# Kernel tuning notes

Measured on AMD Instinct MI355X. Metric: run time of the kernel, lower is better.

## Reference

```python
import jax, jax.numpy as jnp
import numpy as np

K = 1.0          # manifold curvature parameter (Lorentz hyperboloid <x,x>_L = -K)
NUM_HEADS = 16
LN_EPS = 1e-5
MID_EPS = 1e-8


def add_time(space):
    # lift a space-like vector onto the hyperboloid: x0 = sqrt(||s||^2 + K)
    t = jnp.sqrt(jnp.sum(space * space, axis=-1, keepdims=True) + K)
    return jnp.concatenate([t, space], axis=-1)


def hlinear(x, W, b):
    # Lorentz linear: dense map on full ambient vector -> space part, recompute time
    return add_time(jnp.einsum('...d,od->...o', x, W) + b)


def hyp_layernorm(x, g, b):
    s = x[..., 1:]
    mu = jnp.mean(s, axis=-1, keepdims=True)
    var = jnp.mean((s - mu) ** 2, axis=-1, keepdims=True)
    s = (s - mu) * jax.lax.rsqrt(var + LN_EPS) * g + b
    return add_time(s)


def hyp_relu(x):
    return add_time(jax.nn.relu(x[..., 1:]))


def lorentz_norm(v):
    # sqrt(|<v,v>_L|) with clamp for numerical safety
    inner = -v[..., 0] ** 2 + jnp.sum(v[..., 1:] ** 2, axis=-1)
    return jnp.sqrt(jnp.maximum(jnp.abs(inner), MID_EPS))


def midpoint_pair(z, x):
    # manifold.midpoint(stack([z, x], dim=-2)).squeeze(): mean then project back
    ave = 0.5 * (z + x)
    return jnp.sqrt(K) * ave / lorentz_norm(ave)[..., None]


def attention(x, Wq, bq, Wk, bk, Wv, bv, Wo, bo):
    B, S, D = x.shape
    dim = D - 1
    H = NUM_HEADS
    dh = dim // H

    def split_heads(t):
        # drop time, split space into heads, re-lift each head onto hyperboloid
        s = t[..., 1:].reshape(B, S, H, dh).transpose(0, 2, 1, 3)  # [B,H,S,dh]
        return add_time(s)                                          # [B,H,S,dh+1]

    qh = split_heads(hlinear(x, Wq, bq))
    kh = split_heads(hlinear(x, Wk, bk))
    vh = split_heads(hlinear(x, Wv, bv))

    # pairwise Lorentz inner product; scores = -d_L^2 / sqrt(dh)
    inner = (jnp.einsum('bhid,bhjd->bhij', qh[..., 1:], kh[..., 1:])
             - qh[..., 0][..., :, None] * kh[..., 0][..., None, :])
    scores = (2.0 / K + 2.0 * inner) / jnp.sqrt(jnp.asarray(dh, x.dtype))
    att = jax.nn.softmax(scores, axis=-1)

    # Lorentz midpoint aggregation of values (weights sum to 1)
    ave = jnp.einsum('bhij,bhjd->bhid', att, vh)
    out = jnp.sqrt(K) * ave / lorentz_norm(ave)[..., None]  # [B,H,S,dh+1]

    # concat head space parts, re-lift, output projection
    out_space = out[..., 1:].transpose(0, 2, 1, 3).reshape(B, S, dim)
    return hlinear(add_time(out_space), Wo, bo)


def reference(x, Wq, bq, Wk, bk, Wv, bv, Wo, bo, ln1_g, ln1_b, W1, c1, W2, c2, ln2_g, ln2_b):
    z = attention(x, Wq, bq, Wk, bk, Wv, bv, Wo, bo)
    x = midpoint_pair(z, x)
    x = hyp_layernorm(x, ln1_g, ln1_b)
    h = hyp_relu(hlinear(x, W1, c1))
    z = hlinear(h, W2, c2)
    x = midpoint_pair(z, x)
    x = hyp_layernorm(x, ln2_g, ln2_b)
    return x


def setup_inputs() -> dict:
    key = jax.random.key(0)
    ks = jax.random.split(key, 12)
    B, S, dim, mlp = 4, 1024, 1024, 4096
    D = dim + 1
    sc = 0.02
    x = add_time(jax.random.normal(ks[0], (B, S, dim), dtype=jnp.float32))
    return {
        'x': x,
        'Wq': sc * jax.random.normal(ks[1], (dim, D), dtype=jnp.float32),
        'bq': jnp.zeros((dim,), jnp.float32),
        'Wk': sc * jax.random.normal(ks[2], (dim, D), dtype=jnp.float32),
        'bk': jnp.zeros((dim,), jnp.float32),
        'Wv': sc * jax.random.normal(ks[3], (dim, D), dtype=jnp.float32),
        'bv': jnp.zeros((dim,), jnp.float32),
        'Wo': sc * jax.random.normal(ks[4], (dim, D), dtype=jnp.float32),
        'bo': jnp.zeros((dim,), jnp.float32),
        'ln1_g': jnp.ones((dim,), jnp.float32),
        'ln1_b': jnp.zeros((dim,), jnp.float32),
        'W1': sc * jax.random.normal(ks[5], (mlp, D), dtype=jnp.float32),
        'c1': jnp.zeros((mlp,), jnp.float32),
        'W2': sc * jax.random.normal(ks[6], (dim, mlp + 1), dtype=jnp.float32),
        'c2': jnp.zeros((dim,), jnp.float32),
        'ln2_g': jnp.ones((dim,), jnp.float32),
        'ln2_b': jnp.zeros((dim,), jnp.float32),
    }
```

## Files before the change

kernel.cpp:

```cpp
#include <hip/hip_runtime.h>

typedef unsigned short u16;
typedef unsigned int   u32;
typedef short bf16x8 __attribute__((ext_vector_type(8)));
typedef float f32x4  __attribute__((ext_vector_type(4)));

#define NTOK 4096
#define SEQ  1024

__device__ __forceinline__ u16 f2bf(float f){
  union { float f; u32 u; } x; x.f = f;
  u32 r = (x.u + 0x7FFFu + ((x.u >> 16) & 1u)) >> 16;
  return (u16)r;
}
__device__ __forceinline__ float bf2f(u16 u){
  union { u32 u; float f; } x; x.u = ((u32)u) << 16; return x.f;
}
__device__ __forceinline__ void gl_lds16(const void* gp, void* lp){
  __builtin_amdgcn_global_load_lds(
      (const __attribute__((address_space(1))) u32*)gp,
      (__attribute__((address_space(3))) u32*)lp, 16, 0, 0);
}

__global__ __launch_bounds__(256) void conv_x(const float* __restrict__ x,
                                              u16* __restrict__ xs, float* __restrict__ xt){
  int t = blockIdx.x * 256 + threadIdx.x;
  int tok = t >> 10, i = t & 1023;
  xs[t] = f2bf(x[(size_t)tok * 1025 + 1 + i]);
  if (i == 0) xt[tok] = x[(size_t)tok * 1025];
}

__global__ __launch_bounds__(256) void conv_w_all(
    const float* __restrict__ Wq, const float* __restrict__ Wk,
    const float* __restrict__ Wv, const float* __restrict__ Wo,
    const float* __restrict__ W1, const float* __restrict__ W2,
    u16* __restrict__ wqkv, u16* __restrict__ wo_s, u16* __restrict__ w1_s, u16* __restrict__ w2_s,
    float* __restrict__ wqkv0, float* __restrict__ wo0, float* __restrict__ w10, float* __restrict__ w20)
{
  int t = blockIdx.x * 256 + threadIdx.x;
  const int M1 = 1 << 20;
  const float* W; u16* Wb; float* w0; int shift; int idx;
  if (t < 4 * M1){
    int region = t >> 20; idx = t & (M1 - 1); shift = 10;
    if (region == 0)      { W = Wq; Wb = wqkv;          w0 = wqkv0; }
    else if (region == 1) { W = Wk; Wb = wqkv + M1;     w0 = wqkv0 + 1024; }
    else if (region == 2) { W = Wv; Wb = wqkv + 2 * M1; w0 = wqkv0 + 2048; }
    else                  { W = Wo; Wb = wo_s;          w0 = wo0; }
  } else if (t < 8 * M1){
    idx = t - 4 * M1; shift = 10; W = W1; Wb = w1_s; w0 = w10;
  } else {
    idx = t - 8 * M1; shift = 12; W = W2; Wb = w2_s; w0 = w20;
  }
  int Kin = 1 << shift;
  int r = idx >> shift, i = idx & (Kin - 1);
  Wb[idx] = f2bf(W[(size_t)r * (Kin + 1) + 1 + i]);
  if (i == 0) w0[r] = W[(size_t)r * (Kin + 1)];
}

__global__ __launch_bounds__(256) void v_transpose(const u16* __restrict__ qkv,
                                                   const float* __restrict__ vtm,
                                                   u16* __restrict__ vT){
  __shared__ u16 tile[64 * 72];
  const int tid = threadIdx.x;
  const int kt = blockIdx.x, bh = blockIdx.y;
  const int b = bh >> 4, h = bh & 15;
  #pragma unroll
  for (int i = 0; i < 2; i++){
    int c = tid * 2 + i;
    int key = c >> 3, fc = c & 7;
    uint4 v = *(const uint4*)(qkv + ((size_t)(b * 1024 + kt * 64 + key)) * 3072 + 2048 + h * 64 + fc * 8);
    *(uint4*)&tile[key * 72 + fc * 8] = v;
  }
  __syncthreads();
  for (int c = tid; c < 520; c += 256){
    int vtr = c >> 3, kc = c & 7;
    union { uint4 v; u16 s[8]; } d;
    if (vtr == 0){
      #pragma unroll
      for (int j = 0; j < 8; j++) d.s[j] = f2bf(vtm[(size_t)bh * 1024 + kt * 64 + kc * 8 + j]);
    } else {
      int f = vtr - 1;
      #pragma unroll
      for (int j = 0; j < 8; j++) d.s[j] = tile[(kc * 8 + j) * 72 + f];
    }
    *(uint4*)(vT + ((size_t)bh * 65 + vtr) * 1024 + kt * 64 + kc * 8) = d.v;
  }
}

__global__ __launch_bounds__(256) void gemm_bt(
    const u16* __restrict__ A, int lda, const u16* __restrict__ Bm, int ldb,
    const float* __restrict__ at, int at_mode, const float* __restrict__ b0,
    const float* __restrict__ bias_a, const float* __restrict__ bias_b, const float* __restrict__ bias_c,
    u16* __restrict__ Cbf, int ldc, int Kslice, int mode,
    float* __restrict__ qtv, float* __restrict__ ktv, float* __restrict__ vtm,
    float* __restrict__ rowsq)
{
  __shared__ u16 As[2][128 * 64];
  __shared__ u16 Bs[2][128 * 64];
  const int tid = threadIdx.x;
  const int w = tid >> 6, l = tid & 63;
  const int l15 = l & 15, q = l >> 4;
  const int m0 = blockIdx.y * 128, n0 = blockIdx.x * 128;
  const int ks = blockIdx.z;
  const int kbeg = ks * Kslice;
  const int kend = kbeg + Kslice;
  const int wr = w >> 1, wc = w & 1;
  f32x4 acc[4][4] = {};

  auto stage = [&](int kt, int buf){
    #pragma unroll
    for (int half = 0; half < 2; half++){
      #pragma unroll
      for (int i = 0; i < 2; i++){
        int s = (w * 2 + i) * 64 + l;
        int row = s >> 2;
        int kc = ((s & 3) - (s >> 3)) & 3;
        gl_lds16(A  + (size_t)(m0 + row) * lda + kt + half * 32 + kc * 8,
                 &As[buf][half * 4096 + (w * 2 + i) * 512]);
        gl_lds16(Bm + (size_t)(n0 + row) * ldb + kt + half * 32 + kc * 8,
                 &Bs[buf][half * 4096 + (w * 2 + i) * 512]);
      }
    }
  };
  auto compute = [&](int buf, int half){
    bf16x8 af[4], bfr[4];
    #pragma unroll
    for (int i = 0; i < 4; i++){
      int row = wr * 64 + i * 16 + l15;
      int slot = row * 4 + ((q + (row >> 1)) & 3);
      af[i] = *(const bf16x8*)&As[buf][half * 4096 + slot * 8];
    }
    #pragma unroll
    for (int j = 0; j < 4; j++){
      int row = wc * 64 + j * 16 + l15;
      int slot = row * 4 + ((q + (row >> 1)) & 3);
      bfr[j] = *(const bf16x8*)&Bs[buf][half * 4096 + slot * 8];
    }
    #pragma unroll
    for (int i = 0; i < 4; i++)
      #pragma unroll
      for (int j = 0; j < 4; j++)
        acc[i][j] = __builtin_amdgcn_mfma_f32_16x16x32_bf16(af[i], bfr[j], acc[i][j], 0, 0, 0);
  };

  stage(kbeg, 0);
  for (int kt = kbeg; kt < kend; kt += 128){
    __syncthreads();
    if (kt + 64 < kend) stage(kt + 64, 1);
    compute(0, 0); compute(0, 1);
    __syncthreads();
    if (kt + 128 < kend) stage(kt + 128, 0);
    compute(1, 0); compute(1, 1);
  }

  const size_t slice_off = (size_t)ks * (size_t)(gridDim.y * 128) * ldc;
  #pragma unroll
  for (int i = 0; i < 4; i++){
    float atv[4];
    #pragma unroll
    for (int r = 0; r < 4; r++){
      float a = at[m0 + wr * 64 + i * 16 + q * 4 + r];
      atv[r] = at_mode ? sqrtf(a + 1.f) : a;
    }
    float p[4] = {0.f, 0.f, 0.f, 0.f};
    #pragma unroll
    for (int j = 0; j < 4; j++){
      int col = n0 + wc * 64 + j * 16 + l15;
      float b0v = b0[col];
      float bv;
      if (mode == 0) bv = (col < 1024) ? bias_a[col] : (col < 2048) ? bias_b[col - 1024] : bias_c[col - 2048];
      else bv = bias_a[col];
      #pragma unroll
      for (int r = 0; r < 4; r++){
        size_t row = (size_t)(m0 + wr * 64 + i * 16 + q * 4 + r);
        float add = (ks == 0) ? (atv[r] * b0v + bv) : 0.f;
        float v = acc[i][j][r] + add;
        if (mode == 2) v = fmaxf(v, 0.f);
        Cbf[slice_off + row * ldc + col] = f2bf(v);
        if (mode != 1) p[r] += v * v;
      }
    }
    if (mode != 1){
      #pragma unroll
      for (int r = 0; r < 4; r++){
        float s = p[r];
        s += __shfl_xor(s, 1, 64); s += __shfl_xor(s, 2, 64);
        s += __shfl_xor(s, 4, 64); s += __shfl_xor(s, 8, 64);
        if (l15 == 0){
          int row = m0 + wr * 64 + i * 16 + q * 4 + r;
          if (mode == 2){
            atomicAdd(&rowsq[row], s);
          } else {
            int ch = (n0 + wc * 64) >> 6;
            int bb = row >> 10, sidx = row & 1023;
            float t = sqrtf(s + 1.f);
            if (ch < 16)      qtv[((size_t)bb * 16 + ch) * 1024 + sidx] = t;
            else if (ch < 32) ktv[((size_t)bb * 16 + ch - 16) * 1024 + sidx] = t;
            else              vtm[((size_t)bb * 16 + ch - 32) * 1024 + sidx] = t;
          }
        }
      }
    }
  }
}

__global__ __launch_bounds__(512) void attn_kernel(
    const u16* __restrict__ qkv, const float* __restrict__ qt,
    const float* __restrict__ ktm, const u16* __restrict__ vT,
    u16* __restrict__ aout, float* __restrict__ aot_sq)
{
  __shared__ u16 smem[30720];
  u16* Qlds = smem;
  u16* Kl0 = smem + 8192;
  u16* Kl1 = smem + 12288;
  u16* Vl0 = smem + 16384;
  u16* Vl1 = smem;
  u16* Plds = smem + 21504;
  const int tid = threadIdx.x;
  const int w = tid >> 6, l = tid & 63;
  const int l15 = l & 15, qd = l >> 4;
  const int q0 = blockIdx.x * 128;
  const int bh = blockIdx.y;
  const int b = bh >> 4, h = bh & 15;
  const size_t tokbase = (size_t)b << 10;

  #pragma unroll
  for (int i = 0; i < 2; i++){
    int c = i * 512 + w * 64 + l;
    int row = c >> 3, kc = ((c & 7) - row) & 7;
    gl_lds16(qkv + (tokbase + q0 + row) * 3072 + h * 64 + kc * 8, &Qlds[(i * 512 + w * 64) * 8]);
  }
  __syncthreads();
  bf16x8 aq[2];
  {
    int row = w * 16 + l15;
    #pragma unroll
    for (int kk = 0; kk < 2; kk++)
      aq[kk] = *(const bf16x8*)&Qlds[(row * 8 + ((kk * 4 + qd + row) & 7)) * 8];
  }
  float tq[4];
  #pragma unroll
  for (int r = 0; r < 4; r++)
    tq[r] = qt[(size_t)bh * SEQ + q0 + w * 16 + qd * 4 + r];

  auto stage_kv = [&](int kt, int buf){
    u16* K = buf ? Kl1 : Kl0;
    u16* V = buf ? Vl1 : Vl0;
    int c = w * 64 + l;
    int row = c >> 3, kc = ((c & 7) - row) & 7;
    gl_lds16(qkv + (tokbase + kt * 64 + row) * 3072 + 1024 + h * 64 + kc * 8, &K[w * 512]);
    gl_lds16(vT + ((size_t)bh * 65 + row) * 1024 + kt * 64 + kc * 8, &V[w * 512]);
    if (w == 0 && l < 8)
      gl_lds16(vT + ((size_t)bh * 65 + 64) * 1024 + kt * 64 + (l & 7) * 8, &V[4096]);
  };

  float mrow[4] = {-1e30f, -1e30f, -1e30f, -1e30f};
  f32x4 acco[5] = {};

  stage_kv(0, 0);
  for (int kt = 0; kt < 16; kt++){
    __syncthreads();
    if (kt + 1 < 16) stage_kv(kt + 1, (kt + 1) & 1);
    u16* K = (kt & 1) ? Kl1 : Kl0;
    u16* V = (kt & 1) ? Vl1 : Vl0;

    float sc[4][4];
    float mx[4] = {-1e30f, -1e30f, -1e30f, -1e30f};
    #pragma unroll
    for (int ct = 0; ct < 4; ct++){
      f32x4 z = {0.f, 0.f, 0.f, 0.f};
      int key = ct * 16 + l15;
      #pragma unroll
      for (int kk = 0; kk < 2; kk++){
        bf16x8 bk = *(const bf16x8*)&K[(key * 8 + ((kk * 4 + qd + key) & 7)) * 8];
        z = __builtin_amdgcn_mfma_f32_16x16x32_bf16(aq[kk], bk, z, 0, 0, 0);
      }
      float tk = ktm[(size_t)bh * SEQ + kt * 64 + key];
      #pragma unroll
      for (int r = 0; r < 4; r++){
        float s = 0.25f + 0.25f * (z[r] - tq[r] * tk);
        sc[ct][r] = s;
        mx[r] = fmaxf(mx[r], s);
      }
    }
    #pragma unroll
    for (int r = 0; r < 4; r++){
      #pragma unroll
      for (int msk = 1; msk < 16; msk <<= 1)
        mx[r] = fmaxf(mx[r], __shfl_xor(mx[r], msk, 64));
      float mnew = fmaxf(mrow[r], mx[r]);
      float alpha = __expf(mrow[r] - mnew);
      mrow[r] = mnew;
      #pragma unroll
      for (int co = 0; co < 5; co++) acco[co][r] *= alpha;
      mx[r] = mnew;
    }
    #pragma unroll
    for (int ct = 0; ct < 4; ct++)
      #pragma unroll
      for (int r = 0; r < 4; r++)
        Plds[w * 1152 + (qd * 4 + r) * 72 + ct * 16 + l15] = f2bf(__expf(sc[ct][r] - mx[r]));
    asm volatile("s_waitcnt lgkmcnt(0)" ::: "memory");
    bf16x8 ap[2];
    #pragma unroll
    for (int kk = 0; kk < 2; kk++)
      ap[kk] = *(const bf16x8*)&Plds[w * 1152 + l15 * 72 + kk * 32 + qd * 8];
    #pragma unroll
    for (int co = 0; co < 5; co++){
      int vtr = co * 16 + l15;
      #pragma unroll
      for (int kk = 0; kk < 2; kk++){
        bf16x8 bv = *(const bf16x8*)&V[(vtr * 8 + ((kk * 4 + qd + vtr) & 7)) * 8];
        acco[co] = __builtin_amdgcn_mfma_f32_16x16x32_bf16(ap[kk], bv, acco[co], 0, 0, 0);
      }
    }
  }
  #pragma unroll
  for (int r = 0; r < 4; r++){
    float ss = 0.f;
    #pragma unroll
    for (int co = 0; co < 5; co++){
      int col = co * 16 + l15;
      float v = acco[co][r];
      if (col == 0) ss -= v * v;
      else if (col < 65) ss += v * v;
    }
    #pragma unroll
    for (int msk = 1; msk < 16; msk <<= 1) ss += __shfl_xor(ss, msk, 64);
    float v0b = __shfl(acco[0][r], l & 48, 64);
    float sp = ss + v0b * v0b;
    float rn = rsqrtf(fmaxf(fabsf(ss), 1e-8f));
    size_t rowg = tokbase + q0 + w * 16 + qd * 4 + r;
    if (l15 == 0) atomicAdd(&aot_sq[rowg], sp * rn * rn);
    #pragma unroll
    for (int co = 0; co < 5; co++){
      int col = co * 16 + l15;
      if (col >= 1 && col < 65)
        aout[rowg * 1024 + h * 64 + col - 1] = f2bf(acco[co][r] * rn);
    }
  }
}

__device__ __forceinline__ float block_sum(float v, float* red){
  int tid = threadIdx.x;
  #pragma unroll
  for (int m = 1; m < 64; m <<= 1) v += __shfl_xor(v, m, 64);
  __syncthreads();
  if ((tid & 63) == 0) red[tid >> 6] = v;
  __syncthreads();
  return red[0] + red[1] + red[2] + red[3];
}

__global__ __launch_bounds__(256) void mid_ln(
    const u16* __restrict__ z, const u16* __restrict__ xsb, const float* __restrict__ xtv,
    const float* __restrict__ gam, const float* __restrict__ bet,
    u16* __restrict__ ob, float* __restrict__ ot,
    float* __restrict__ ofull, int mode_out, int nsl)
{
  __shared__ float red[4];
  const int tid = threadIdx.x;
  const int tok = blockIdx.x;
  float zv[4], xv[4], xtime;
  xtime = xtv[tok];
  {
    const u16* xr = xsb + (size_t)tok * 1024;
    #pragma unroll
    for (int j = 0; j < 4; j++) xv[j] = bf2f(xr[tid + j * 256]);
  }
  {
    #pragma unroll
    for (int j = 0; j < 4; j++) zv[j] = 0.f;
    for (int s = 0; s < nsl; s++){
      const u16* zs = z + (size_t)s * NTOK * 1024 + (size_t)tok * 1024;
      #pragma unroll
      for (int j = 0; j < 4; j++) zv[j] += bf2f(zs[tid + j * 256]);
    }
  }
  float ssz = 0.f;
  #pragma unroll
  for (int j = 0; j < 4; j++) ssz += zv[j] * zv[j];
  ssz = block_sum(ssz, red);
  float tz = sqrtf(ssz + 1.f);
  float av[4]; float ssa = 0.f;
  #pragma unroll
  for (int j = 0; j < 4; j++){ av[j] = 0.5f * (zv[j] + xv[j]); ssa += av[j] * av[j]; }
  ssa = block_sum(ssa, red);
  float avt = 0.5f * (tz + xtime);
  float rn = rsqrtf(fmaxf(fabsf(ssa - avt * avt), 1e-8f));
  float uv[4]; float su = 0.f, squ = 0.f;
  #pragma unroll
  for (int j = 0; j < 4; j++){ uv[j] = av[j] * rn; su += uv[j]; squ += uv[j] * uv[j]; }
  su = block_sum(su, red);
  squ = block_sum(squ, red);
  float mu = su * (1.f / 1024.f);
  float var = squ * (1.f / 1024.f) - mu * mu;
  float rv = rsqrtf(fmaxf(var, 0.f) + 1e-5f);
  float sv[4]; float sss = 0.f;
  #pragma unroll
  for (int j = 0; j < 4; j++){
    int i = tid + j * 256;
    sv[j] = (uv[j] - mu) * rv * gam[i] + bet[i];
    sss += sv[j] * sv[j];
  }
  sss = block_sum(sss, red);
  float tout = sqrtf(sss + 1.f);
  if (mode_out == 0){
    #pragma unroll
    for (int j = 0; j < 4; j++){
      int i = tid + j * 256;
      ob[(size_t)tok * 1024 + i] = f2bf(sv[j]);
    }
    if (tid == 0) ot[tok] = tout;
  } else {
    float* orow = ofull + (size_t)tok * 1025;
    #pragma unroll
    for (int j = 0; j < 4; j++) orow[1 + tid + j * 256] = sv[j];
    if (tid == 0) orow[0] = tout;
  }
}

extern "C" void kernel_launch(void* const* d_in, const int* in_sizes, int n_in,
                              void* d_out, int out_size, void* d_ws, size_t ws_size,
                              hipStream_t stream){
  const float* x   = (const float*)d_in[0];
  const float* Wq  = (const float*)d_in[1];
  const float* bq  = (const float*)d_in[2];
  const float* Wk  = (const float*)d_in[3];
  const float* bk  = (const float*)d_in[4];
  const float* Wv  = (const float*)d_in[5];
  const float* bv  = (const float*)d_in[6];
  const float* Wo  = (const float*)d_in[7];
  const float* bo  = (const float*)d_in[8];
  const float* g1  = (const float*)d_in[9];
  const float* be1 = (const float*)d_in[10];
  const float* W1  = (const float*)d_in[11];
  const float* c1  = (const float*)d_in[12];
  const float* W2  = (const float*)d_in[13];
  const float* c2  = (const float*)d_in[14];
  const float* g2  = (const float*)d_in[15];
  const float* be2 = (const float*)d_in[16];
  float* out = (float*)d_out;

  char* p = (char*)d_ws;
  auto take = [&](size_t n){ char* r = p; p += (n + 255) & ~(size_t)255; return r; };
  u16*   xs    = (u16*)  take((size_t)NTOK * 1024 * 2);
  float* xt    = (float*)take(NTOK * 4);
  u16*   wqkv  = (u16*)  take((size_t)3072 * 1024 * 2);
  float* wqkv0 = (float*)take(3072 * 4);
  u16*   wo_s  = (u16*)  take((size_t)1024 * 1024 * 2);
  float* wo0   = (float*)take(1024 * 4);
  u16*   w1_s  = (u16*)  take((size_t)4096 * 1024 * 2);
  float* w10   = (float*)take(4096 * 4);
  u16*   w2_s  = (u16*)  take((size_t)1024 * 4096 * 2);
  float* w20   = (float*)take(1024 * 4);
  u16*   qkvb  = (u16*)  take((size_t)NTOK * 3072 * 2);
  float* qtv   = (float*)take((size_t)64 * 1024 * 4);
  float* ktv   = (float*)take((size_t)64 * 1024 * 4);
  float* vtm   = (float*)take((size_t)64 * 1024 * 4);
  u16*   vT    = (u16*)  take((size_t)64 * 65 * 1024 * 2);
  u16*   aoutb = (u16*)  take((size_t)NTOK * 1024 * 2);
  float* sqbuf = (float*)take((size_t)2 * NTOK * 4);
  float* aot_sq = sqbuf;
  float* htv_sq = sqbuf + NTOK;
  u16*   zbuf  = (u16*)  take((size_t)4 * NTOK * 1024 * 2);
  u16*   x1b   = (u16*)  take((size_t)NTOK * 1024 * 2);
  float* x1t   = (float*)take(NTOK * 4);
  u16*   hbuf  = (u16*)  take((size_t)NTOK * 4096 * 2);

  hipMemsetAsync(sqbuf, 0, (size_t)2 * NTOK * 4, stream);

  conv_x<<<NTOK * 1024 / 256, 256, 0, stream>>>(x, xs, xt);
  conv_w_all<<<(12 * 1024 * 1024) / 256, 256, 0, stream>>>(
      Wq, Wk, Wv, Wo, W1, W2, wqkv, wo_s, w1_s, w2_s, wqkv0, wo0, w10, w20);

  gemm_bt<<<dim3(24, 32), 256, 0, stream>>>(xs, 1024, wqkv, 1024, xt, 0, wqkv0,
      bq, bk, bv, qkvb, 3072, 1024, 0, qtv, ktv, vtm, nullptr);
  v_transpose<<<dim3(16, 64), 256, 0, stream>>>(qkvb, vtm, vT);
  attn_kernel<<<dim3(8, 64), 512, 0, stream>>>(qkvb, qtv, ktv, vT, aoutb, aot_sq);
  gemm_bt<<<dim3(8, 32, 2), 256, 0, stream>>>(aoutb, 1024, wo_s, 1024, aot_sq, 1, wo0,
      bo, nullptr, nullptr, zbuf, 1024, 512, 1, nullptr, nullptr, nullptr, nullptr);
  mid_ln<<<NTOK, 256, 0, stream>>>(zbuf, xs, xt, g1, be1,
      x1b, x1t, nullptr, 0, 2);
  gemm_bt<<<dim3(32, 32), 256, 0, stream>>>(x1b, 1024, w1_s, 1024, x1t, 0, w10,
      c1, nullptr, nullptr, hbuf, 4096, 1024, 2, nullptr, nullptr, nullptr, htv_sq);
  gemm_bt<<<dim3(8, 32, 4), 256, 0, stream>>>(hbuf, 4096, w2_s, 4096, htv_sq, 1, w20,
      c2, nullptr, nullptr, zbuf, 1024, 1024, 1, nullptr, nullptr, nullptr, nullptr);
  mid_ln<<<NTOK, 256, 0, stream>>>(zbuf, x1b, x1t, g2, be2,
      nullptr, nullptr, out, 1, 4);
}
```

Before: 431.2 us.

## Give each wave private LDS tiles and replace block barriers with waitcnt pipelining

The GEMM now has each wave stage its own 64-row A slice and 64-row B slice into a private LDS region. This removes the block-wide __syncthreads, and manual s_waitcnt vmcnt/lgkmcnt counters order the double-buffered K=32 stages. The aim is to remove barrier stalls and let waves run independently. In exchange, each A and B row slice is loaded twice (waves sharing wr or wc duplicate loads), which doubles global and LDS fill traffic, and the stage depth per iteration shrinks from 64 to 32.

```diff
diff --git a/kernel.cpp b/kernel.cpp
--- a/kernel.cpp
+++ b/kernel.cpp
@@ -95,62 +95,63 @@
     float* __restrict__ qtv, float* __restrict__ ktv, float* __restrict__ vtm,
     float* __restrict__ rowsq)
 {
-  __shared__ u16 As[2][128 * 64];
-  __shared__ u16 Bs[2][128 * 64];
+  __shared__ u16 lds[4 * 2 * 2 * 2048];
   const int tid = threadIdx.x;
   const int w = tid >> 6, l = tid & 63;
   const int l15 = l & 15, q = l >> 4;
   const int m0 = blockIdx.y * 128, n0 = blockIdx.x * 128;
   const int ks = blockIdx.z;
   const int kbeg = ks * Kslice;
-  const int kend = kbeg + Kslice;
   const int wr = w >> 1, wc = w & 1;
+  u16* base = &lds[w * 8192];
   f32x4 acc[4][4] = {};
 
   auto stage = [&](int kt, int buf){
     #pragma unroll
-    for (int half = 0; half < 2; half++){
-      #pragma unroll
-      for (int i = 0; i < 2; i++){
-        int s = (w * 2 + i) * 64 + l;
-        int row = s >> 2;
-        int kc = ((s & 3) - (s >> 3)) & 3;
-        gl_lds16(A  + (size_t)(m0 + row) * lda + kt + half * 32 + kc * 8,
-                 &As[buf][half * 4096 + (w * 2 + i) * 512]);
-        gl_lds16(Bm + (size_t)(n0 + row) * ldb + kt + half * 32 + kc * 8,
-                 &Bs[buf][half * 4096 + (w * 2 + i) * 512]);
-      }
+    for (int i = 0; i < 4; i++){
+      int s = i * 64 + l;
+      int row = s >> 2;
+      int kc = ((s & 3) - (s >> 3)) & 3;
+      gl_lds16(A + (size_t)(m0 + wr * 64 + row) * lda + kt + kc * 8,
+               &base[(buf * 2 + 0) * 2048 + i * 512]);
+    }
+    #pragma unroll
+    for (int i = 0; i < 4; i++){
+      int s = i * 64 + l;
+      int row = s >> 2;
+      int kc = ((s & 3) - (s >> 3)) & 3;
+      gl_lds16(Bm + (size_t)(n0 + wc * 64 + row) * ldb + kt + kc * 8,
+               &base[(buf * 2 + 1) * 2048 + i * 512]);
     }
   };
-  auto compute = [&](int buf, int half){
+
+  const int nst = Kslice >> 5;
+  stage(kbeg, 0);
+  stage(kbeg + 32, 1);
+  for (int j = 0; j < nst; j++){
+    if (j + 1 < nst) asm volatile("s_waitcnt vmcnt(8)" ::: "memory");
+    else             asm volatile("s_waitcnt vmcnt(0)" ::: "memory");
+    const int buf = j & 1;
     bf16x8 af[4], bfr[4];
     #pragma unroll
     for (int i = 0; i < 4; i++){
-      int row = wr * 64 + i * 16 + l15;
+      int row = i * 16 + l15;
       int slot = row * 4 + ((q + (row >> 1)) & 3);
-      af[i] = *(const bf16x8*)&As[buf][half * 4096 + slot * 8];
-    }
-    #pragma unroll
-    for (int j = 0; j < 4; j++){
-      int row = wc * 64 + j * 16 + l15;
+      af[i] = *(const bf16x8*)&base[(buf * 2 + 0) * 2048 + slot * 8];
+    }
+    #pragma unroll
+    for (int i = 0; i < 4; i++){
+      int row = i * 16 + l15;
       int slot = row * 4 + ((q + (row >> 1)) & 3);
-      bfr[j] = *(const bf16x8*)&Bs[buf][half * 4096 + slot * 8];
-    }
+      bfr[i] = *(const bf16x8*)&base[(buf * 2 + 1) * 2048 + slot * 8];
+    }
+    asm volatile("s_waitcnt lgkmcnt(0)" ::: "memory");
+    if (j + 2 < nst) stage(kbeg + (j + 2) * 32, buf);
     #pragma unroll
     for (int i = 0; i < 4; i++)
       #pragma unroll
-      for (int j = 0; j < 4; j++)
-        acc[i][j] = __builtin_amdgcn_mfma_f32_16x16x32_bf16(af[i], bfr[j], acc[i][j], 0, 0, 0);
-  };
-
-  stage(kbeg, 0);
-  for (int kt = kbeg; kt < kend; kt += 128){
-    __syncthreads();
-    if (kt + 64 < kend) stage(kt + 64, 1);
-    compute(0, 0); compute(0, 1);
-    __syncthreads();
-    if (kt + 128 < kend) stage(kt + 128, 0);
-    compute(1, 0); compute(1, 1);
+      for (int jj = 0; jj < 4; jj++)
+        acc[i][jj] = __builtin_amdgcn_mfma_f32_16x16x32_bf16(af[i], bfr[jj], acc[i][jj], 0, 0, 0);
   }
 
   const size_t slice_off = (size_t)ks * (size_t)(gridDim.y * 128) * ldc;
```

Measured after the change: 459.4 us. +6.5%, slower.
